# Optimization experiments

Measured on AMD Instinct MI355X. Metric: run time of the kernel, lower is better.

Reference implementation:

```python
import jax, jax.numpy as jnp
import numpy as np

N_NODES = 50000
N_EDGES = 800000
NODE_DIM = 128
EDGE_DIM = 10
IN_DIM = 2 * NODE_DIM + EDGE_DIM
BN_EPS = 1e-5


def setup_inputs() -> dict:
    key = jax.random.key(0)
    ks = jax.random.split(key, 8)
    h = jax.random.normal(ks[0], (N_NODES, NODE_DIM), dtype=jnp.float32)
    edge_index = jax.random.randint(ks[1], (2, N_EDGES), 0, N_NODES, dtype=jnp.int64)
    edge_feat = jax.random.normal(ks[2], (N_EDGES, EDGE_DIM), dtype=jnp.float32)
    scale = 1.0 / np.sqrt(IN_DIM)
    gate_w = jax.random.normal(ks[3], (IN_DIM, NODE_DIM), dtype=jnp.float32) * scale
    gate_b = jax.random.normal(ks[4], (NODE_DIM,), dtype=jnp.float32) * scale
    cand_w = jax.random.normal(ks[5], (IN_DIM, NODE_DIM), dtype=jnp.float32) * scale
    cand_b = jax.random.normal(ks[6], (NODE_DIM,), dtype=jnp.float32) * scale
    bn_gamma = jnp.ones((NODE_DIM,), dtype=jnp.float32)
    bn_beta = jnp.zeros((NODE_DIM,), dtype=jnp.float32)
    return {"h": h, "edge_index": edge_index, "edge_feat": edge_feat,
            "gate_w": gate_w, "gate_b": gate_b, "cand_w": cand_w, "cand_b": cand_b,
            "bn_gamma": bn_gamma, "bn_beta": bn_beta}


def reference(h, edge_index, edge_feat, gate_w, gate_b, cand_w, cand_b, bn_gamma, bn_beta):
    src = edge_index[0]
    dst = edge_index[1]
    # gather endpoint features and concat with edge features: [E, 2*D + De]
    z = jnp.concatenate([h[src], h[dst], edge_feat], axis=1)
    g = jax.nn.sigmoid(z @ gate_w + gate_b)   # [E, D]
    c = jax.nn.softplus(z @ cand_w + cand_b)  # [E, D]
    m = g * c
    # scatter-add messages to source nodes (matches index_add_(0, src, m))
    agg = jax.ops.segment_sum(m, src, num_segments=h.shape[0])
    # BatchNorm1d in training mode: batch mean / biased variance over nodes
    mean = jnp.mean(agg, axis=0)
    var = jnp.var(agg, axis=0)
    agg_bn = (agg - mean) * jax.lax.rsqrt(var + BN_EPS) * bn_gamma + bn_beta
    return jax.nn.softplus(h + agg_bn)
```

## Files before the change

### kernel.cpp

```cpp
#include <hip/hip_runtime.h>
#include <math.h>

#define N_NODES 50000
#define N_EDGES 800000
#define D 128
#define DE 10
#define TE 64
#define N_TILES (N_EDGES / TE)
#define SST 132
#define ASTR 136
#define OST 520
#define WP2_ELEMS (4 * 32 * 64 * 8)
#define WEF_ELEMS (16 * 64 * 8)
#define SCAN_BLOCKS 196
#define CSTRIDE 16

typedef __bf16 bf16x8 __attribute__((ext_vector_type(8)));
typedef __bf16 bf16x4 __attribute__((ext_vector_type(4)));
typedef __bf16 bf16x2 __attribute__((ext_vector_type(2)));
typedef float  f32x4  __attribute__((ext_vector_type(4)));

__device__ __forceinline__ float fast_sigmoid(float x) {
    float t = __builtin_amdgcn_exp2f(-1.44269504089f * x);
    return __builtin_amdgcn_rcpf(1.0f + t);
}
__device__ __forceinline__ float fast_softplus(float x) {
    float t = __builtin_amdgcn_exp2f(-1.44269504089f * fabsf(x));
    return fmaxf(x, 0.0f) + 0.69314718056f * __builtin_amdgcn_logf(1.0f + t);
}

__global__ __launch_bounds__(256) void prep(
    const float* __restrict__ gw, const float* __restrict__ cw,
    const int* __restrict__ ei,
    __bf16* __restrict__ wp2, __bf16* __restrict__ wef,
    int* __restrict__ counts)
{
    int bx = blockIdx.x, t = threadIdx.x;
    if (bx < 256) {
        int idx = bx * 256 + t;
        int j    = idx & 7;
        int lane = (idx >> 3) & 63;
        int nb   = (idx >> 9) & 31;
        int kb   = idx >> 14;
        int k    = kb * 32 + ((lane >> 4) << 3) + j;
        int jp   = nb * 16 + (lane & 15);
        float v;
        if      (jp < 128) v = gw[k * D + jp];
        else if (jp < 256) v = cw[k * D + (jp - 128)];
        else if (jp < 384) v = gw[(128 + k) * D + (jp - 256)];
        else               v = cw[(128 + k) * D + (jp - 384)];
        wp2[idx] = (__bf16)v;
    } else if (bx < 288) {
        int idx = (bx - 256) * 256 + t;
        int j    = idx & 7;
        int lane = (idx >> 3) & 63;
        int nb   = idx >> 9;
        int k    = ((lane >> 4) << 3) + j;
        int col  = (nb >> 1) * 16 + (lane & 15);
        const float* w = (nb & 1) ? cw : gw;
        wef[idx] = (__bf16)((k < 10) ? w[(256 + k) * D + col] : 0.0f);
    } else {
        int e = (bx - 288) * 256 + t;
        atomicAdd(&counts[ei[e] * CSTRIDE], 1);
    }
}

__global__ __launch_bounds__(256) void scan_partials(
    const int* __restrict__ counts, int* __restrict__ bsum)
{
    __shared__ int ss[256];
    int t = threadIdx.x;
    int i = blockIdx.x * 256 + t;
    int c = (i < N_NODES) ? counts[i * CSTRIDE] : 0;
    ss[t] = c;
    __syncthreads();
    #pragma unroll
    for (int off = 1; off < 256; off <<= 1) {
        int v = (t >= off) ? ss[t - off] : 0;
        __syncthreads();
        ss[t] += v;
        __syncthreads();
    }
    if (t == 255) bsum[blockIdx.x] = ss[255];
}

__global__ __launch_bounds__(256) void scan_final(
    int* __restrict__ counts, const int* __restrict__ bsum)
{
    __shared__ int sb[256];
    __shared__ int ss[256];
    int t = threadIdx.x;
    sb[t] = (t < SCAN_BLOCKS) ? bsum[t] : 0;
    int i = blockIdx.x * 256 + t;
    int c = (i < N_NODES) ? counts[i * CSTRIDE] : 0;
    ss[t] = c;
    __syncthreads();
    #pragma unroll
    for (int off = 1; off < 256; off <<= 1) {
        int v  = (t >= off) ? ss[t - off] : 0;
        int vb = (t >= off) ? sb[t - off] : 0;
        __syncthreads();
        ss[t] += v;
        sb[t] += vb;
        __syncthreads();
    }
    int base = blockIdx.x ? sb[blockIdx.x - 1] : 0;
    if (i < N_NODES) counts[i * CSTRIDE] = base + ss[t] - c;
}

__global__ __launch_bounds__(256) void csr_scatter(
    const int* __restrict__ ei, int* __restrict__ cursor,
    int2* __restrict__ sde)
{
    int e = blockIdx.x * 256 + threadIdx.x;
    int node = ei[e];
    int pos = atomicAdd(&cursor[node * CSTRIDE], 1);
    sde[pos] = make_int2(node | (ei[N_EDGES + e] << 16), e);
}

__global__ __launch_bounds__(512, 4) void node_gemm(
    const float* __restrict__ h, const __bf16* __restrict__ wp2,
    __bf16* __restrict__ pa, __bf16* __restrict__ pb)
{
    __shared__ __align__(16) __bf16 sm[64 * OST];
    __bf16* za = sm;
    const int t  = threadIdx.x;
    const int r0 = blockIdx.x * 64;

    #pragma unroll
    for (int it = 0; it < 4; ++it) {
        int ch  = it * 512 + t;
        int row = ch >> 5, cs = ch & 31;
        int node = r0 + row;
        float4 v = (node < N_NODES) ? *(const float4*)&h[(size_t)node * D + cs * 4]
                                    : make_float4(0.f, 0.f, 0.f, 0.f);
        bf16x4 o = { (__bf16)v.x, (__bf16)v.y, (__bf16)v.z, (__bf16)v.w };
        *(bf16x4*)&za[row * ASTR + cs * 4] = o;
    }
    __syncthreads();

    const int w = t >> 6, l = t & 63, quad = l >> 4, col16 = l & 15;
    f32x4 acc[4][4];
    #pragma unroll
    for (int mt = 0; mt < 4; ++mt)
        #pragma unroll
        for (int nt = 0; nt < 4; ++nt)
            acc[mt][nt] = (f32x4)0.0f;

    const __bf16* zp = &za[col16 * ASTR + quad * 8];
    const __bf16* bp = &wp2[(size_t)((w * 4) * 64 + l) * 8];

    #pragma unroll
    for (int kb = 0; kb < 4; ++kb) {
        bf16x8 afr[4];
        #pragma unroll
        for (int mt = 0; mt < 4; ++mt)
            afr[mt] = *(const bf16x8*)&zp[mt * 16 * ASTR + kb * 32];
        bf16x8 bfr[4];
        #pragma unroll
        for (int nt = 0; nt < 4; ++nt)
            bfr[nt] = *(const bf16x8*)&bp[(size_t)(kb * 32 + nt) * 512];
        #pragma unroll
        for (int mt = 0; mt < 4; ++mt)
            #pragma unroll
            for (int nt = 0; nt < 4; ++nt)
                acc[mt][nt] = __builtin_amdgcn_mfma_f32_16x16x32_bf16(
                    afr[mt], bfr[nt], acc[mt][nt], 0, 0, 0);
    }
    __syncthreads();

    #pragma unroll
    for (int mt = 0; mt < 4; ++mt)
        #pragma unroll
        for (int nt = 0; nt < 4; ++nt)
            #pragma unroll
            for (int r = 0; r < 4; ++r) {
                int row  = mt * 16 + quad * 4 + r;
                int colj = (w * 4 + nt) * 16 + col16;
                sm[row * OST + colj] = (__bf16)acc[mt][nt][r];
            }
    __syncthreads();

    #pragma unroll
    for (int it = 0; it < 8; ++it) {
        int ch  = it * 512 + t;
        int row = ch >> 6, cc = ch & 63;
        int node = r0 + row;
        if (node < N_NODES) {
            bf16x8 v = *(const bf16x8*)&sm[row * OST + cc * 8];
            int j0 = cc * 8;
            if (j0 < 256) *(bf16x8*)&pa[(size_t)node * 256 + j0]         = v;
            else          *(bf16x8*)&pb[(size_t)node * 256 + (j0 - 256)] = v;
        }
    }
}

__global__ __launch_bounds__(512, 6) void edge_fuse(
    const __bf16* __restrict__ pa, const __bf16* __restrict__ pb,
    const int2* __restrict__ sde, const float* __restrict__ ef,
    const __bf16* __restrict__ wef,
    const float* __restrict__ gb, const float* __restrict__ cb,
    float* __restrict__ agg)
{
    __shared__ __align__(16) unsigned int sbuf[TE * SST];
    __shared__ __align__(16) __bf16 zE[TE * 32];
    __shared__ int s_src[TE], s_dst[TE], s_eid[TE];

    const int t  = threadIdx.x;
    const int e0 = blockIdx.x * TE;
    const int w = t >> 6, l = t & 63, quad = l >> 4, col16 = l & 15;

    const __bf16* wpp = &wef[(size_t)((w * 2) * 64 + l) * 8];
    bf16x8 bfr0 = *(const bf16x8*)&wpp[0];
    bf16x8 bfr1 = *(const bf16x8*)&wpp[512];
    const int c = w * 16 + col16;
    const float gbv = gb[c], cbv = cb[c];

    if (t < TE) {
        int2 p = sde[e0 + t];
        s_src[t] = p.x & 0xFFFF;
        s_dst[t] = (p.x >> 16) & 0xFFFF;
        s_eid[t] = p.y;
    }
    __syncthreads();

    if (t < TE) {
        const float* efr = &ef[(size_t)s_eid[t] * DE];
        __bf16* row = &zE[t * 32];
        #pragma unroll
        for (int j = 0; j < 5; ++j) {
            float2 a = *(const float2*)&efr[j * 2];
            bf16x2 p = { (__bf16)a.x, (__bf16)a.y };
            *(bf16x2*)&row[j * 2] = p;
        }
        *(bf16x2*)&row[10] = (bf16x2)(__bf16)0.0f;
        *(bf16x4*)&row[12] = (bf16x4)(__bf16)0.0f;
        *(bf16x8*)&row[16] = (bf16x8)(__bf16)0.0f;
        *(bf16x8*)&row[24] = (bf16x8)(__bf16)0.0f;
    }

    #pragma unroll
    for (int it = 0; it < 2; ++it) {
        int id  = it * 512 + t;
        int e   = id >> 4, grp = id & 15;
        int src = s_src[e], dst = s_dst[e];
        int c0  = grp * 8;
        bf16x8 ag = *(const bf16x8*)&pa[(size_t)src * 256 + c0];
        bf16x8 ac = *(const bf16x8*)&pa[(size_t)src * 256 + 128 + c0];
        bf16x8 bg = *(const bf16x8*)&pb[(size_t)dst * 256 + c0];
        bf16x8 bc = *(const bf16x8*)&pb[(size_t)dst * 256 + 128 + c0];
        unsigned int wds[8];
        #pragma unroll
        for (int j = 0; j < 8; ++j) {
            float gs = (float)ag[j] + (float)bg[j];
            float cs = (float)ac[j] + (float)bc[j];
            bf16x2 pr = { (__bf16)gs, (__bf16)cs };
            wds[j] = __builtin_bit_cast(unsigned int, pr);
        }
        *(uint4*)&sbuf[e * SST + c0]     = *(const uint4*)&wds[0];
        *(uint4*)&sbuf[e * SST + c0 + 4] = *(const uint4*)&wds[4];
    }
    __syncthreads();

    f32x4 acc[4][2];
    #pragma unroll
    for (int mt = 0; mt < 4; ++mt) {
        const bf16x8 a = *(const bf16x8*)&zE[(mt * 16 + col16) * 32 + quad * 8];
        acc[mt][0] = __builtin_amdgcn_mfma_f32_16x16x32_bf16(a, bfr0, (f32x4)0.0f, 0, 0, 0);
        acc[mt][1] = __builtin_amdgcn_mfma_f32_16x16x32_bf16(a, bfr1, (f32x4)0.0f, 0, 0, 0);
    }

    #pragma unroll
    for (int mt = 0; mt < 4; ++mt) {
        #pragma unroll
        for (int r = 0; r < 4; ++r) {
            int e = mt * 16 + quad * 4 + r;
            unsigned int u = sbuf[e * SST + c];
            float gs = __builtin_bit_cast(float, u << 16);
            float cs = __builtin_bit_cast(float, u & 0xFFFF0000u);
            float sg = fast_sigmoid(acc[mt][0][r] + gs + gbv);
            float sp = fast_softplus(acc[mt][1][r] + cs + cbv);
            ((float*)sbuf)[e * SST + c] = sg * sp;
        }
    }
    __syncthreads();

    const int seg = t >> 7;
    const int cc  = t & 127;
    const int rlo = seg * 16, rhi = rlo + 16;
    int   cur = s_src[rlo];
    float s   = 0.0f;
    const float* ms = (const float*)sbuf;
    for (int e = rlo; e < rhi; ++e) {
        int node = s_src[e];
        float v  = ms[e * SST + cc];
        if (node != cur) {
            atomicAdd(&agg[(size_t)cur * D + cc], s);
            s = 0.0f; cur = node;
        }
        s += v;
    }
    atomicAdd(&agg[(size_t)cur * D + cc], s);
}

__global__ __launch_bounds__(256) void col_stats(
    const float* __restrict__ agg, float* __restrict__ stats)
{
    const int t    = threadIdx.x;
    const int col  = t & 127;
    const int half = t >> 7;
    float s = 0.0f, s2 = 0.0f;
    for (int r = blockIdx.x * 2 + half; r < N_NODES; r += gridDim.x * 2) {
        float v = agg[(size_t)r * D + col];
        s += v; s2 += v * v;
    }
    atomicAdd(&stats[col], s);
    atomicAdd(&stats[128 + col], s2);
}

__global__ __launch_bounds__(256) void out_softplus(
    const float* __restrict__ h, const float* __restrict__ agg,
    const float* __restrict__ stats, const float* __restrict__ gamma,
    const float* __restrict__ beta, float* __restrict__ out)
{
    __shared__ float sc[128], bi[128];
    int t = threadIdx.x;
    if (t < 128) {
        const float inv_n = 1.0f / (float)N_NODES;
        float mean = stats[t] * inv_n;
        float var  = stats[128 + t] * inv_n - mean * mean;
        var = fmaxf(var, 0.0f);
        float rstd = rsqrtf(var + 1e-5f);
        float s = rstd * gamma[t];
        sc[t] = s;
        bi[t] = beta[t] - mean * s;
    }
    __syncthreads();
    int idx4 = blockIdx.x * 256 + t;
    int base = idx4 * 4;
    if (base < N_NODES * D) {
        float4 hv = *(const float4*)&h[base];
        float4 av = *(const float4*)&agg[base];
        int c = base & 127;
        float4 o;
        o.x = fast_softplus(hv.x + av.x * sc[c + 0] + bi[c + 0]);
        o.y = fast_softplus(hv.y + av.y * sc[c + 1] + bi[c + 1]);
        o.z = fast_softplus(hv.z + av.z * sc[c + 2] + bi[c + 2]);
        o.w = fast_softplus(hv.w + av.w * sc[c + 3] + bi[c + 3]);
        *(float4*)&out[base] = o;
    }
}

extern "C" void kernel_launch(void* const* d_in, const int* in_sizes, int n_in,
                              void* d_out, int out_size, void* d_ws, size_t ws_size,
                              hipStream_t stream) {
    const float* h     = (const float*)d_in[0];
    const int*   ei    = (const int*)  d_in[1];
    const float* ef    = (const float*)d_in[2];
    const float* gw    = (const float*)d_in[3];
    const float* gb    = (const float*)d_in[4];
    const float* cw    = (const float*)d_in[5];
    const float* cb    = (const float*)d_in[6];
    const float* gamma = (const float*)d_in[7];
    const float* beta  = (const float*)d_in[8];
    float* out = (float*)d_out;

    float*  agg    = (float*)d_ws;
    float*  stats  = agg + (size_t)N_NODES * D;
    int*    counts = (int*)(stats + 256);
    int*    bsum   = counts + N_NODES * CSTRIDE;
    __bf16* pb     = (__bf16*)counts;
    char*   afterU = (char*)counts + (size_t)N_NODES * 256 * sizeof(__bf16);
    __bf16* wp2    = (__bf16*)afterU;
    __bf16* wef    = wp2 + WP2_ELEMS;
    int2*   sde    = (int2*)(wef + WEF_ELEMS);
    __bf16* pa     = (__bf16*)d_out;

    const size_t zero_bytes = ((size_t)N_NODES * D + 256) * sizeof(float)
                            + (size_t)N_NODES * CSTRIDE * sizeof(int);
    hipMemsetAsync(d_ws, 0, zero_bytes, stream);
    prep<<<3413, 256, 0, stream>>>(gw, cw, ei, wp2, wef, counts);
    scan_partials<<<SCAN_BLOCKS, 256, 0, stream>>>(counts, bsum);
    scan_final<<<SCAN_BLOCKS, 256, 0, stream>>>(counts, bsum);
    csr_scatter<<<N_EDGES / 256, 256, 0, stream>>>(ei, counts, sde);
    node_gemm<<<(N_NODES + 63) / 64, 512, 0, stream>>>(h, wp2, pa, pb);
    edge_fuse<<<N_TILES, 512, 0, stream>>>(pa, pb, sde, ef, wef, gb, cb, agg);
    col_stats<<<784, 256, 0, stream>>>(agg, stats);
    out_softplus<<<(N_NODES * D / 4 + 255) / 256, 256, 0, stream>>>(
        h, agg, stats, gamma, beta, out);
}
```

Baseline: 375.8 us.

## Replace edge-tiled MFMA fuse with per-node CSR wavefront aggregation without atomics

```diff
diff --git a/kernel.cpp b/kernel.cpp
--- a/kernel.cpp
+++ b/kernel.cpp
@@ -5,15 +5,11 @@
 #define N_EDGES 800000
 #define D 128
 #define DE 10
-#define TE 64
-#define N_TILES (N_EDGES / TE)
-#define SST 132
+#define WP2_ELEMS (4 * 32 * 64 * 8)
+#define SCAN_BLOCKS 196
+#define CSTRIDE 16
 #define ASTR 136
 #define OST 520
-#define WP2_ELEMS (4 * 32 * 64 * 8)
-#define WEF_ELEMS (16 * 64 * 8)
-#define SCAN_BLOCKS 196
-#define CSTRIDE 16
 
 typedef __bf16 bf16x8 __attribute__((ext_vector_type(8)));
 typedef __bf16 bf16x4 __attribute__((ext_vector_type(4)));
@@ -28,12 +24,17 @@
     float t = __builtin_amdgcn_exp2f(-1.44269504089f * fabsf(x));
     return fmaxf(x, 0.0f) + 0.69314718056f * __builtin_amdgcn_logf(1.0f + t);
 }
+__device__ __forceinline__ float2 bf2f(unsigned int u) {
+    float2 r;
+    r.x = __builtin_bit_cast(float, u << 16);
+    r.y = __builtin_bit_cast(float, u & 0xFFFF0000u);
+    return r;
+}
 
 __global__ __launch_bounds__(256) void prep(
     const float* __restrict__ gw, const float* __restrict__ cw,
     const int* __restrict__ ei,
-    __bf16* __restrict__ wp2, __bf16* __restrict__ wef,
-    int* __restrict__ counts)
+    __bf16* __restrict__ wp2, int* __restrict__ counts)
 {
     int bx = blockIdx.x, t = threadIdx.x;
     if (bx < 256) {
@@ -50,17 +51,8 @@
         else if (jp < 384) v = gw[(128 + k) * D + (jp - 256)];
         else               v = cw[(128 + k) * D + (jp - 384)];
         wp2[idx] = (__bf16)v;
-    } else if (bx < 288) {
-        int idx = (bx - 256) * 256 + t;
-        int j    = idx & 7;
-        int lane = (idx >> 3) & 63;
-        int nb   = idx >> 9;
-        int k    = ((lane >> 4) << 3) + j;
-        int col  = (nb >> 1) * 16 + (lane & 15);
-        const float* w = (nb & 1) ? cw : gw;
-        wef[idx] = (__bf16)((k < 10) ? w[(256 + k) * D + col] : 0.0f);
     } else {
-        int e = (bx - 288) * 256 + t;
+        int e = (bx - 256) * 256 + t;
         atomicAdd(&counts[ei[e] * CSTRIDE], 1);
     }
 }
@@ -85,7 +77,8 @@
 }
 
 __global__ __launch_bounds__(256) void scan_final(
-    int* __restrict__ counts, const int* __restrict__ bsum)
+    int* __restrict__ counts, const int* __restrict__ bsum,
+    int* __restrict__ rp)
 {
     __shared__ int sb[256];
     __shared__ int ss[256];
@@ -105,7 +98,12 @@
         __syncthreads();
     }
     int base = blockIdx.x ? sb[blockIdx.x - 1] : 0;
-    if (i < N_NODES) counts[i * CSTRIDE] = base + ss[t] - c;
+    if (i < N_NODES) {
+        int excl = base + ss[t] - c;
+        counts[i * CSTRIDE] = excl;
+        rp[i] = excl;
+    }
+    if (blockIdx.x == 0 && t == 0) rp[N_NODES] = N_EDGES;
 }
 
 __global__ __launch_bounds__(256) void csr_scatter(
@@ -115,7 +113,7 @@
     int e = blockIdx.x * 256 + threadIdx.x;
     int node = ei[e];
     int pos = atomicAdd(&cursor[node * CSTRIDE], 1);
-    sde[pos] = make_int2(node | (ei[N_EDGES + e] << 16), e);
+    sde[pos] = make_int2(ei[N_EDGES + e], e);
 }
 
 __global__ __launch_bounds__(512, 4) void node_gemm(
@@ -195,112 +193,66 @@
     }
 }
 
-__global__ __launch_bounds__(512, 6) void edge_fuse(
+__global__ __launch_bounds__(256, 6) void node_fuse(
     const __bf16* __restrict__ pa, const __bf16* __restrict__ pb,
     const int2* __restrict__ sde, const float* __restrict__ ef,
-    const __bf16* __restrict__ wef,
+    const int* __restrict__ rp,
+    const float* __restrict__ gw, const float* __restrict__ cw,
     const float* __restrict__ gb, const float* __restrict__ cb,
     float* __restrict__ agg)
 {
-    __shared__ __align__(16) unsigned int sbuf[TE * SST];
-    __shared__ __align__(16) __bf16 zE[TE * 32];
-    __shared__ int s_src[TE], s_dst[TE], s_eid[TE];
-
-    const int t  = threadIdx.x;
-    const int e0 = blockIdx.x * TE;
-    const int w = t >> 6, l = t & 63, quad = l >> 4, col16 = l & 15;
-
-    const __bf16* wpp = &wef[(size_t)((w * 2) * 64 + l) * 8];
-    bf16x8 bfr0 = *(const bf16x8*)&wpp[0];
-    bf16x8 bfr1 = *(const bf16x8*)&wpp[512];
-    const int c = w * 16 + col16;
-    const float gbv = gb[c], cbv = cb[c];
-
-    if (t < TE) {
-        int2 p = sde[e0 + t];
-        s_src[t] = p.x & 0xFFFF;
-        s_dst[t] = (p.x >> 16) & 0xFFFF;
-        s_eid[t] = p.y;
-    }
-    __syncthreads();
-
-    if (t < TE) {
-        const float* efr = &ef[(size_t)s_eid[t] * DE];
-        __bf16* row = &zE[t * 32];
-        #pragma unroll
-        for (int j = 0; j < 5; ++j) {
-            float2 a = *(const float2*)&efr[j * 2];
-            bf16x2 p = { (__bf16)a.x, (__bf16)a.y };
-            *(bf16x2*)&row[j * 2] = p;
+    const int t = threadIdx.x;
+    const int w = t >> 6, l = t & 63;
+    const int n = blockIdx.x * 4 + w;
+    const int c0 = 2 * l;
+
+    int beg = __builtin_amdgcn_readfirstlane(rp[n]);
+    int end = __builtin_amdgcn_readfirstlane(rp[n + 1]);
+
+    float2 ag = bf2f(*(const unsigned int*)&pa[(size_t)n * 256 + c0]);
+    float2 ac = bf2f(*(const unsigned int*)&pa[(size_t)n * 256 + 128 + c0]);
+
+    float4 wk[10];
+    #pragma unroll
+    for (int k = 0; k < 10; ++k) {
+        float2 g = *(const float2*)&gw[(size_t)(256 + k) * D + c0];
+        float2 c = *(const float2*)&cw[(size_t)(256 + k) * D + c0];
+        wk[k] = make_float4(g.x, g.y, c.x, c.y);
+    }
+    const float gb0 = gb[c0], gb1 = gb[c0 + 1];
+    const float cb0 = cb[c0], cb1 = cb[c0 + 1];
+
+    float acc0 = 0.0f, acc1 = 0.0f;
+
+    int2 rec = (beg < end) ? sde[beg] : make_int2(0, 0);
+    for (int i = beg; i < end; ++i) {
+        const int dst = __builtin_amdgcn_readfirstlane(rec.x);
+        const int eid = __builtin_amdgcn_readfirstlane(rec.y);
+        int2 nrec = (i + 1 < end) ? sde[i + 1] : rec;
+
+        unsigned int ugb = *(const unsigned int*)&pb[(size_t)dst * 256 + c0];
+        unsigned int ucb = *(const unsigned int*)&pb[(size_t)dst * 256 + 128 + c0];
+
+        const float* efr = &ef[(size_t)eid * DE];
+        float4 d = make_float4(gb0, gb1, cb0, cb1);
+        #pragma unroll
+        for (int k = 0; k < 10; ++k) {
+            float e = efr[k];
+            d.x = fmaf(e, wk[k].x, d.x);
+            d.y = fmaf(e, wk[k].y, d.y);
+            d.z = fmaf(e, wk[k].z, d.z);
+            d.w = fmaf(e, wk[k].w, d.w);
         }
-        *(bf16x2*)&row[10] = (bf16x2)(__bf16)0.0f;
-        *(bf16x4*)&row[12] = (bf16x4)(__bf16)0.0f;
-        *(bf16x8*)&row[16] = (bf16x8)(__bf16)0.0f;
-        *(bf16x8*)&row[24] = (bf16x8)(__bf16)0.0f;
-    }
-
-    #pragma unroll
-    for (int it = 0; it < 2; ++it) {
-        int id  = it * 512 + t;
-        int e   = id >> 4, grp = id & 15;
-        int src = s_src[e], dst = s_dst[e];
-        int c0  = grp * 8;
-        bf16x8 ag = *(const bf16x8*)&pa[(size_t)src * 256 + c0];
-        bf16x8 ac = *(const bf16x8*)&pa[(size_t)src * 256 + 128 + c0];
-        bf16x8 bg = *(const bf16x8*)&pb[(size_t)dst * 256 + c0];
-        bf16x8 bc = *(const bf16x8*)&pb[(size_t)dst * 256 + 128 + c0];
-        unsigned int wds[8];
-        #pragma unroll
-        for (int j = 0; j < 8; ++j) {
-            float gs = (float)ag[j] + (float)bg[j];
-            float cs = (float)ac[j] + (float)bc[j];
-            bf16x2 pr = { (__bf16)gs, (__bf16)cs };
-            wds[j] = __builtin_bit_cast(unsigned int, pr);
-        }
-        *(uint4*)&sbuf[e * SST + c0]     = *(const uint4*)&wds[0];
-        *(uint4*)&sbuf[e * SST + c0 + 4] = *(const uint4*)&wds[4];
-    }
-    __syncthreads();
-
-    f32x4 acc[4][2];
-    #pragma unroll
-    for (int mt = 0; mt < 4; ++mt) {
-        const bf16x8 a = *(const bf16x8*)&zE[(mt * 16 + col16) * 32 + quad * 8];
-        acc[mt][0] = __builtin_amdgcn_mfma_f32_16x16x32_bf16(a, bfr0, (f32x4)0.0f, 0, 0, 0);
-        acc[mt][1] = __builtin_amdgcn_mfma_f32_16x16x32_bf16(a, bfr1, (f32x4)0.0f, 0, 0, 0);
-    }
-
-    #pragma unroll
-    for (int mt = 0; mt < 4; ++mt) {
-        #pragma unroll
-        for (int r = 0; r < 4; ++r) {
-            int e = mt * 16 + quad * 4 + r;
-            unsigned int u = sbuf[e * SST + c];
-            float gs = __builtin_bit_cast(float, u << 16);
-            float cs = __builtin_bit_cast(float, u & 0xFFFF0000u);
-            float sg = fast_sigmoid(acc[mt][0][r] + gs + gbv);
-            float sp = fast_softplus(acc[mt][1][r] + cs + cbv);
-            ((float*)sbuf)[e * SST + c] = sg * sp;
-        }
-    }
-    __syncthreads();
-
-    const int seg = t >> 7;
-    const int cc  = t & 127;
-    const int rlo = seg * 16, rhi = rlo + 16;
-    int   cur = s_src[rlo];
-    float s   = 0.0f;
-    const float* ms = (const float*)sbuf;
-    for (int e = rlo; e < rhi; ++e) {
-        int node = s_src[e];
-        float v  = ms[e * SST + cc];
-        if (node != cur) {
-            atomicAdd(&agg[(size_t)cur * D + cc], s);
-            s = 0.0f; cur = node;
-        }
-        s += v;
-    }
-    atomicAdd(&agg[(size_t)cur * D + cc], s);
+        float2 bg = bf2f(ugb), bc = bf2f(ucb);
+        float g0 = ag.x + bg.x + d.x;
+        float g1 = ag.y + bg.y + d.y;
+        float x0 = ac.x + bc.x + d.z;
+        float x1 = ac.y + bc.y + d.w;
+        acc0 += fast_sigmoid(g0) * fast_softplus(x0);
+        acc1 += fast_sigmoid(g1) * fast_softplus(x1);
+        rec = nrec;
+    }
+    *(float2*)&agg[(size_t)n * D + c0] = make_float2(acc0, acc1);
 }
 
 __global__ __launch_bounds__(256) void col_stats(
@@ -372,20 +324,18 @@
     __bf16* pb     = (__bf16*)counts;
     char*   afterU = (char*)counts + (size_t)N_NODES * 256 * sizeof(__bf16);
     __bf16* wp2    = (__bf16*)afterU;
-    __bf16* wef    = wp2 + WP2_ELEMS;
-    int2*   sde    = (int2*)(wef + WEF_ELEMS);
+    int2*   sde    = (int2*)(wp2 + WP2_ELEMS);
+    int*    rp     = (int*)(sde + N_EDGES);
     __bf16* pa     = (__bf16*)d_out;
 
-    const size_t zero_bytes = ((size_t)N_NODES * D + 256) * sizeof(float)
-                            + (size_t)N_NODES * CSTRIDE * sizeof(int);
-    hipMemsetAsync(d_ws, 0, zero_bytes, stream);
-    prep<<<3413, 256, 0, stream>>>(gw, cw, ei, wp2, wef, counts);
+    hipMemsetAsync(stats, 0, 256 * sizeof(float) + (size_t)N_NODES * CSTRIDE * sizeof(int), stream);
+    prep<<<3381, 256, 0, stream>>>(gw, cw, ei, wp2, counts);
     scan_partials<<<SCAN_BLOCKS, 256, 0, stream>>>(counts, bsum);
-    scan_final<<<SCAN_BLOCKS, 256, 0, stream>>>(counts, bsum);
+    scan_final<<<SCAN_BLOCKS, 256, 0, stream>>>(counts, bsum, rp);
     csr_scatter<<<N_EDGES / 256, 256, 0, stream>>>(ei, counts, sde);
     node_gemm<<<(N_NODES + 63) / 64, 512, 0, stream>>>(h, wp2, pa, pb);
-    edge_fuse<<<N_TILES, 512, 0, stream>>>(pa, pb, sde, ef, wef, gb, cb, agg);
+    node_fuse<<<N_NODES / 4, 256, 0, stream>>>(pa, pb, sde, ef, rp, gw, cw, gb, cb, agg);
     col_stats<<<784, 256, 0, stream>>>(agg, stats);
-    out_softplus<<<(N_NODES * D / 4 + 255) / 256, 256, 0, stream>>>(
+    out_softplus<<<N_NODES * D / 4 / 256, 256, 0, stream>>>(
         h, agg, stats, gamma, beta, out);
 }
```

Result: slower. 426.8 us (+13.6%).

## Merge CSR build and BN finish stages into cooperative grid-synced kernels

Applied to the files above, without the earlier changes.

```diff
diff --git a/kernel.cpp b/kernel.cpp
--- a/kernel.cpp
+++ b/kernel.cpp
@@ -1,5 +1,8 @@
 #include <hip/hip_runtime.h>
+#include <hip/hip_cooperative_groups.h>
 #include <math.h>
+
+namespace cg = cooperative_groups;
 
 #define N_NODES 50000
 #define N_EDGES 800000
@@ -14,6 +17,7 @@
 #define WEF_ELEMS (16 * 64 * 8)
 #define SCAN_BLOCKS 196
 #define CSTRIDE 16
+#define ZERO_F4 1800064
 
 typedef __bf16 bf16x8 __attribute__((ext_vector_type(8)));
 typedef __bf16 bf16x4 __attribute__((ext_vector_type(4)));
@@ -29,15 +33,22 @@
     return fmaxf(x, 0.0f) + 0.69314718056f * __builtin_amdgcn_logf(1.0f + t);
 }
 
-__global__ __launch_bounds__(256) void prep(
+__global__ __launch_bounds__(256) void build_csr(
     const float* __restrict__ gw, const float* __restrict__ cw,
     const int* __restrict__ ei,
     __bf16* __restrict__ wp2, __bf16* __restrict__ wef,
-    int* __restrict__ counts)
+    int* __restrict__ counts, int* __restrict__ bsum,
+    int2* __restrict__ sde, float4* __restrict__ zbase)
 {
-    int bx = blockIdx.x, t = threadIdx.x;
-    if (bx < 256) {
-        int idx = bx * 256 + t;
+    cg::grid_group grid = cg::this_grid();
+    const int t = threadIdx.x, b = blockIdx.x;
+    const int gtid = b * 256 + t;
+    const int gstride = SCAN_BLOCKS * 256;
+
+    const float4 z4 = make_float4(0.f, 0.f, 0.f, 0.f);
+    for (int i = gtid; i < ZERO_F4; i += gstride)
+        zbase[i] = z4;
+    for (int idx = gtid; idx < WP2_ELEMS; idx += gstride) {
         int j    = idx & 7;
         int lane = (idx >> 3) & 63;
         int nb   = (idx >> 9) & 31;
@@ -50,8 +61,9 @@
         else if (jp < 384) v = gw[(128 + k) * D + (jp - 256)];
         else               v = cw[(128 + k) * D + (jp - 384)];
         wp2[idx] = (__bf16)v;
-    } else if (bx < 288) {
-        int idx = (bx - 256) * 256 + t;
+    }
+    if (gtid < WEF_ELEMS) {
+        int idx = gtid;
         int j    = idx & 7;
         int lane = (idx >> 3) & 63;
         int nb   = idx >> 9;
@@ -59,19 +71,18 @@
         int col  = (nb >> 1) * 16 + (lane & 15);
         const float* w = (nb & 1) ? cw : gw;
         wef[idx] = (__bf16)((k < 10) ? w[(256 + k) * D + col] : 0.0f);
-    } else {
-        int e = (bx - 288) * 256 + t;
+    }
+    grid.sync();
+
+    #pragma unroll 4
+    for (int e = gtid; e < N_EDGES; e += gstride)
         atomicAdd(&counts[ei[e] * CSTRIDE], 1);
-    }
-}
-
-__global__ __launch_bounds__(256) void scan_partials(
-    const int* __restrict__ counts, int* __restrict__ bsum)
-{
+    grid.sync();
+
     __shared__ int ss[256];
-    int t = threadIdx.x;
-    int i = blockIdx.x * 256 + t;
-    int c = (i < N_NODES) ? counts[i * CSTRIDE] : 0;
+    __shared__ int sb[256];
+    const int i = b * 256 + t;
+    const int c = (i < N_NODES) ? counts[i * CSTRIDE] : 0;
     ss[t] = c;
     __syncthreads();
     #pragma unroll
@@ -81,41 +92,28 @@
         ss[t] += v;
         __syncthreads();
     }
-    if (t == 255) bsum[blockIdx.x] = ss[255];
-}
-
-__global__ __launch_bounds__(256) void scan_final(
-    int* __restrict__ counts, const int* __restrict__ bsum)
-{
-    __shared__ int sb[256];
-    __shared__ int ss[256];
-    int t = threadIdx.x;
+    if (t == 255) bsum[b] = ss[255];
+    grid.sync();
+
     sb[t] = (t < SCAN_BLOCKS) ? bsum[t] : 0;
-    int i = blockIdx.x * 256 + t;
-    int c = (i < N_NODES) ? counts[i * CSTRIDE] : 0;
-    ss[t] = c;
     __syncthreads();
     #pragma unroll
     for (int off = 1; off < 256; off <<= 1) {
-        int v  = (t >= off) ? ss[t - off] : 0;
-        int vb = (t >= off) ? sb[t - off] : 0;
+        int v = (t >= off) ? sb[t - off] : 0;
         __syncthreads();
-        ss[t] += v;
-        sb[t] += vb;
+        sb[t] += v;
         __syncthreads();
     }
-    int base = blockIdx.x ? sb[blockIdx.x - 1] : 0;
+    int base = b ? sb[b - 1] : 0;
     if (i < N_NODES) counts[i * CSTRIDE] = base + ss[t] - c;
-}
-
-__global__ __launch_bounds__(256) void csr_scatter(
-    const int* __restrict__ ei, int* __restrict__ cursor,
-    int2* __restrict__ sde)
-{
-    int e = blockIdx.x * 256 + threadIdx.x;
-    int node = ei[e];
-    int pos = atomicAdd(&cursor[node * CSTRIDE], 1);
-    sde[pos] = make_int2(node | (ei[N_EDGES + e] << 16), e);
+    grid.sync();
+
+    #pragma unroll 4
+    for (int e = gtid; e < N_EDGES; e += gstride) {
+        int node = ei[e];
+        int pos = atomicAdd(&counts[node * CSTRIDE], 1);
+        sde[pos] = make_int2(node | (ei[N_EDGES + e] << 16), e);
+    }
 }
 
 __global__ __launch_bounds__(512, 4) void node_gemm(
@@ -303,28 +301,28 @@
     atomicAdd(&agg[(size_t)cur * D + cc], s);
 }
 
-__global__ __launch_bounds__(256) void col_stats(
-    const float* __restrict__ agg, float* __restrict__ stats)
-{
-    const int t    = threadIdx.x;
-    const int col  = t & 127;
-    const int half = t >> 7;
-    float s = 0.0f, s2 = 0.0f;
-    for (int r = blockIdx.x * 2 + half; r < N_NODES; r += gridDim.x * 2) {
-        float v = agg[(size_t)r * D + col];
-        s += v; s2 += v * v;
-    }
-    atomicAdd(&stats[col], s);
-    atomicAdd(&stats[128 + col], s2);
-}
-
-__global__ __launch_bounds__(256) void out_softplus(
+__global__ __launch_bounds__(256) void finish(
     const float* __restrict__ h, const float* __restrict__ agg,
-    const float* __restrict__ stats, const float* __restrict__ gamma,
+    float* __restrict__ stats, const float* __restrict__ gamma,
     const float* __restrict__ beta, float* __restrict__ out)
 {
+    cg::grid_group grid = cg::this_grid();
+    const int t = threadIdx.x;
+
+    {
+        const int col  = t & 127;
+        const int half = t >> 7;
+        float s = 0.0f, s2 = 0.0f;
+        for (int r = blockIdx.x * 2 + half; r < N_NODES; r += gridDim.x * 2) {
+            float v = agg[(size_t)r * D + col];
+            s += v; s2 += v * v;
+        }
+        atomicAdd(&stats[col], s);
+        atomicAdd(&stats[128 + col], s2);
+    }
+    grid.sync();
+
     __shared__ float sc[128], bi[128];
-    int t = threadIdx.x;
     if (t < 128) {
         const float inv_n = 1.0f / (float)N_NODES;
         float mean = stats[t] * inv_n;
@@ -336,17 +334,17 @@
         bi[t] = beta[t] - mean * s;
     }
     __syncthreads();
-    int idx4 = blockIdx.x * 256 + t;
-    int base = idx4 * 4;
-    if (base < N_NODES * D) {
+    const int total4 = N_NODES * D / 4;
+    for (int idx4 = blockIdx.x * 256 + t; idx4 < total4; idx4 += gridDim.x * 256) {
+        int base = idx4 * 4;
         float4 hv = *(const float4*)&h[base];
         float4 av = *(const float4*)&agg[base];
-        int c = base & 127;
+        int cc = base & 127;
         float4 o;
-        o.x = fast_softplus(hv.x + av.x * sc[c + 0] + bi[c + 0]);
-        o.y = fast_softplus(hv.y + av.y * sc[c + 1] + bi[c + 1]);
-        o.z = fast_softplus(hv.z + av.z * sc[c + 2] + bi[c + 2]);
-        o.w = fast_softplus(hv.w + av.w * sc[c + 3] + bi[c + 3]);
+        o.x = fast_softplus(hv.x + av.x * sc[cc + 0] + bi[cc + 0]);
+        o.y = fast_softplus(hv.y + av.y * sc[cc + 1] + bi[cc + 1]);
+        o.z = fast_softplus(hv.z + av.z * sc[cc + 2] + bi[cc + 2]);
+        o.w = fast_softplus(hv.w + av.w * sc[cc + 3] + bi[cc + 3]);
         *(float4*)&out[base] = o;
     }
 }
@@ -375,17 +373,21 @@
     __bf16* wef    = wp2 + WP2_ELEMS;
     int2*   sde    = (int2*)(wef + WEF_ELEMS);
     __bf16* pa     = (__bf16*)d_out;
-
-    const size_t zero_bytes = ((size_t)N_NODES * D + 256) * sizeof(float)
-                            + (size_t)N_NODES * CSTRIDE * sizeof(int);
-    hipMemsetAsync(d_ws, 0, zero_bytes, stream);
-    prep<<<3413, 256, 0, stream>>>(gw, cw, ei, wp2, wef, counts);
-    scan_partials<<<SCAN_BLOCKS, 256, 0, stream>>>(counts, bsum);
-    scan_final<<<SCAN_BLOCKS, 256, 0, stream>>>(counts, bsum);
-    csr_scatter<<<N_EDGES / 256, 256, 0, stream>>>(ei, counts, sde);
+    float4* zbase  = (float4*)d_ws;
+
+    {
+        void* args[] = { (void*)&gw, (void*)&cw, (void*)&ei, (void*)&wp2,
+                         (void*)&wef, (void*)&counts, (void*)&bsum,
+                         (void*)&sde, (void*)&zbase };
+        hipLaunchCooperativeKernel((const void*)build_csr,
+                                   dim3(SCAN_BLOCKS), dim3(256), args, 0, stream);
+    }
     node_gemm<<<(N_NODES + 63) / 64, 512, 0, stream>>>(h, wp2, pa, pb);
     edge_fuse<<<N_TILES, 512, 0, stream>>>(pa, pb, sde, ef, wef, gb, cb, agg);
-    col_stats<<<784, 256, 0, stream>>>(agg, stats);
-    out_softplus<<<(N_NODES * D / 4 + 255) / 256, 256, 0, stream>>>(
-        h, agg, stats, gamma, beta, out);
-}
+    {
+        void* args[] = { (void*)&h, (void*)&agg, (void*)&stats,
+                         (void*)&gamma, (void*)&beta, (void*)&out };
+        hipLaunchCooperativeKernel((const void*)finish,
+                                   dim3(784), dim3(256), args, 0, stream);
+    }
+}
```

After: 519.9 us. 38.3% more time.

## Replace atomic CSR scatter with rank-based permutation and interleave gate/cand projections

Applied to the files above, without the earlier changes.

```diff
diff --git a/kernel.cpp b/kernel.cpp
--- a/kernel.cpp
+++ b/kernel.cpp
@@ -14,6 +14,8 @@
 #define WEF_ELEMS (16 * 64 * 8)
 #define SCAN_BLOCKS 196
 #define CSTRIDE 16
+#define SCAT_BLOCKS 1563
+#define GEMM_BLOCKS 782
 
 typedef __bf16 bf16x8 __attribute__((ext_vector_type(8)));
 typedef __bf16 bf16x4 __attribute__((ext_vector_type(4)));
@@ -28,12 +30,18 @@
     float t = __builtin_amdgcn_exp2f(-1.44269504089f * fabsf(x));
     return fmaxf(x, 0.0f) + 0.69314718056f * __builtin_amdgcn_logf(1.0f + t);
 }
+__device__ __forceinline__ float bflo(unsigned int u) {
+    return __builtin_bit_cast(float, u << 16);
+}
+__device__ __forceinline__ float bfhi(unsigned int u) {
+    return __builtin_bit_cast(float, u & 0xFFFF0000u);
+}
 
 __global__ __launch_bounds__(256) void prep(
     const float* __restrict__ gw, const float* __restrict__ cw,
     const int* __restrict__ ei,
     __bf16* __restrict__ wp2, __bf16* __restrict__ wef,
-    int* __restrict__ counts)
+    int* __restrict__ counts, unsigned short* __restrict__ rank)
 {
     int bx = blockIdx.x, t = threadIdx.x;
     if (bx < 256) {
@@ -61,7 +69,8 @@
         wef[idx] = (__bf16)((k < 10) ? w[(256 + k) * D + col] : 0.0f);
     } else {
         int e = (bx - 288) * 256 + t;
-        atomicAdd(&counts[ei[e] * CSTRIDE], 1);
+        int r = atomicAdd(&counts[ei[e] * CSTRIDE], 1);
+        rank[e] = (unsigned short)r;
     }
 }
 
@@ -85,7 +94,8 @@
 }
 
 __global__ __launch_bounds__(256) void scan_final(
-    int* __restrict__ counts, const int* __restrict__ bsum)
+    const int* __restrict__ counts, const int* __restrict__ bsum,
+    int* __restrict__ excl)
 {
     __shared__ int sb[256];
     __shared__ int ss[256];
@@ -105,27 +115,28 @@
         __syncthreads();
     }
     int base = blockIdx.x ? sb[blockIdx.x - 1] : 0;
-    if (i < N_NODES) counts[i * CSTRIDE] = base + ss[t] - c;
-}
-
-__global__ __launch_bounds__(256) void csr_scatter(
-    const int* __restrict__ ei, int* __restrict__ cursor,
-    int2* __restrict__ sde)
-{
-    int e = blockIdx.x * 256 + threadIdx.x;
-    int node = ei[e];
-    int pos = atomicAdd(&cursor[node * CSTRIDE], 1);
-    sde[pos] = make_int2(node | (ei[N_EDGES + e] << 16), e);
-}
-
-__global__ __launch_bounds__(512, 4) void node_gemm(
+    if (i < N_NODES) excl[i] = base + ss[t] - c;
+}
+
+__global__ __launch_bounds__(512, 4) void scatter_gemm(
+    const int* __restrict__ ei, const unsigned short* __restrict__ rank,
+    const int* __restrict__ excl, int* __restrict__ perm,
     const float* __restrict__ h, const __bf16* __restrict__ wp2,
-    __bf16* __restrict__ pa, __bf16* __restrict__ pb)
-{
+    unsigned int* __restrict__ paI, unsigned int* __restrict__ pbI)
+{
+    if (blockIdx.x < SCAT_BLOCKS) {
+        int e = blockIdx.x * 512 + threadIdx.x;
+        if (e < N_EDGES) {
+            int node = ei[e];
+            perm[excl[node] + (int)rank[e]] = e;
+        }
+        return;
+    }
+
     __shared__ __align__(16) __bf16 sm[64 * OST];
     __bf16* za = sm;
     const int t  = threadIdx.x;
-    const int r0 = blockIdx.x * 64;
+    const int r0 = (blockIdx.x - SCAT_BLOCKS) * 64;
 
     #pragma unroll
     for (int it = 0; it < 4; ++it) {
@@ -183,28 +194,38 @@
 
     #pragma unroll
     for (int it = 0; it < 8; ++it) {
-        int ch  = it * 512 + t;
-        int row = ch >> 6, cc = ch & 63;
+        int ch   = it * 512 + t;
+        int row  = ch >> 6;
+        int sub  = ch & 63;
+        int hp   = sub >> 5;
+        int c0   = (sub & 31) * 4;
         int node = r0 + row;
         if (node < N_NODES) {
-            bf16x8 v = *(const bf16x8*)&sm[row * OST + cc * 8];
-            int j0 = cc * 8;
-            if (j0 < 256) *(bf16x8*)&pa[(size_t)node * 256 + j0]         = v;
-            else          *(bf16x8*)&pb[(size_t)node * 256 + (j0 - 256)] = v;
+            const __bf16* sr = &sm[row * OST + hp * 256];
+            bf16x4 gl = *(const bf16x4*)&sr[c0];
+            bf16x4 cl = *(const bf16x4*)&sr[128 + c0];
+            unsigned int wds[4];
+            #pragma unroll
+            for (int i = 0; i < 4; ++i) {
+                bf16x2 pr = { gl[i], cl[i] };
+                wds[i] = __builtin_bit_cast(unsigned int, pr);
+            }
+            unsigned int* dp = hp ? pbI : paI;
+            *(uint4*)&dp[(size_t)node * 128 + c0] = *(const uint4*)&wds[0];
         }
     }
 }
 
 __global__ __launch_bounds__(512, 6) void edge_fuse(
-    const __bf16* __restrict__ pa, const __bf16* __restrict__ pb,
-    const int2* __restrict__ sde, const float* __restrict__ ef,
-    const __bf16* __restrict__ wef,
+    const unsigned int* __restrict__ paI, const unsigned int* __restrict__ pbI,
+    const int* __restrict__ perm, const int* __restrict__ ei,
+    const float* __restrict__ ef, const __bf16* __restrict__ wef,
     const float* __restrict__ gb, const float* __restrict__ cb,
     float* __restrict__ agg)
 {
-    __shared__ __align__(16) unsigned int sbuf[TE * SST];
+    __shared__ __align__(16) float ms[TE * SST];
     __shared__ __align__(16) __bf16 zE[TE * 32];
-    __shared__ int s_src[TE], s_dst[TE], s_eid[TE];
+    __shared__ int s_src[TE], s_dst[TE];
 
     const int t  = threadIdx.x;
     const int e0 = blockIdx.x * TE;
@@ -217,49 +238,22 @@
     const float gbv = gb[c], cbv = cb[c];
 
     if (t < TE) {
-        int2 p = sde[e0 + t];
-        s_src[t] = p.x & 0xFFFF;
-        s_dst[t] = (p.x >> 16) & 0xFFFF;
-        s_eid[t] = p.y;
-    }
-    __syncthreads();
-
-    if (t < TE) {
-        const float* efr = &ef[(size_t)s_eid[t] * DE];
+        int p = perm[e0 + t];
+        s_src[t] = ei[p];
+        s_dst[t] = ei[N_EDGES + p];
+        const float* efr = &ef[(size_t)p * DE];
         __bf16* row = &zE[t * 32];
         #pragma unroll
         for (int j = 0; j < 5; ++j) {
             float2 a = *(const float2*)&efr[j * 2];
-            bf16x2 p = { (__bf16)a.x, (__bf16)a.y };
-            *(bf16x2*)&row[j * 2] = p;
+            bf16x2 pr = { (__bf16)a.x, (__bf16)a.y };
+            *(bf16x2*)&row[j * 2] = pr;
         }
         *(bf16x2*)&row[10] = (bf16x2)(__bf16)0.0f;
         *(bf16x4*)&row[12] = (bf16x4)(__bf16)0.0f;
         *(bf16x8*)&row[16] = (bf16x8)(__bf16)0.0f;
         *(bf16x8*)&row[24] = (bf16x8)(__bf16)0.0f;
     }
-
-    #pragma unroll
-    for (int it = 0; it < 2; ++it) {
-        int id  = it * 512 + t;
-        int e   = id >> 4, grp = id & 15;
-        int src = s_src[e], dst = s_dst[e];
-        int c0  = grp * 8;
-        bf16x8 ag = *(const bf16x8*)&pa[(size_t)src * 256 + c0];
-        bf16x8 ac = *(const bf16x8*)&pa[(size_t)src * 256 + 128 + c0];
-        bf16x8 bg = *(const bf16x8*)&pb[(size_t)dst * 256 + c0];
-        bf16x8 bc = *(const bf16x8*)&pb[(size_t)dst * 256 + 128 + c0];
-        unsigned int wds[8];
-        #pragma unroll
-        for (int j = 0; j < 8; ++j) {
-            float gs = (float)ag[j] + (float)bg[j];
-            float cs = (float)ac[j] + (float)bc[j];
-            bf16x2 pr = { (__bf16)gs, (__bf16)cs };
-            wds[j] = __builtin_bit_cast(unsigned int, pr);
-        }
-        *(uint4*)&sbuf[e * SST + c0]     = *(const uint4*)&wds[0];
-        *(uint4*)&sbuf[e * SST + c0 + 4] = *(const uint4*)&wds[4];
-    }
     __syncthreads();
 
     f32x4 acc[4][2];
@@ -272,15 +266,19 @@
 
     #pragma unroll
     for (int mt = 0; mt < 4; ++mt) {
+        unsigned int uA[4], uB[4];
         #pragma unroll
         for (int r = 0; r < 4; ++r) {
             int e = mt * 16 + quad * 4 + r;
-            unsigned int u = sbuf[e * SST + c];
-            float gs = __builtin_bit_cast(float, u << 16);
-            float cs = __builtin_bit_cast(float, u & 0xFFFF0000u);
-            float sg = fast_sigmoid(acc[mt][0][r] + gs + gbv);
-            float sp = fast_softplus(acc[mt][1][r] + cs + cbv);
-            ((float*)sbuf)[e * SST + c] = sg * sp;
+            uA[r] = paI[(size_t)s_src[e] * 128 + c];
+            uB[r] = pbI[(size_t)s_dst[e] * 128 + c];
+        }
+        #pragma unroll
+        for (int r = 0; r < 4; ++r) {
+            int e = mt * 16 + quad * 4 + r;
+            float g = bflo(uA[r]) + bflo(uB[r]) + acc[mt][0][r] + gbv;
+            float x = bfhi(uA[r]) + bfhi(uB[r]) + acc[mt][1][r] + cbv;
+            ms[e * SST + c] = fast_sigmoid(g) * fast_softplus(x);
         }
     }
     __syncthreads();
@@ -290,7 +288,6 @@
     const int rlo = seg * 16, rhi = rlo + 16;
     int   cur = s_src[rlo];
     float s   = 0.0f;
-    const float* ms = (const float*)sbuf;
     for (int e = rlo; e < rhi; ++e) {
         int node = s_src[e];
         float v  = ms[e * SST + cc];
@@ -365,27 +362,29 @@
     const float* beta  = (const float*)d_in[8];
     float* out = (float*)d_out;
 
-    float*  agg    = (float*)d_ws;
-    float*  stats  = agg + (size_t)N_NODES * D;
-    int*    counts = (int*)(stats + 256);
-    int*    bsum   = counts + N_NODES * CSTRIDE;
-    __bf16* pb     = (__bf16*)counts;
-    char*   afterU = (char*)counts + (size_t)N_NODES * 256 * sizeof(__bf16);
-    __bf16* wp2    = (__bf16*)afterU;
-    __bf16* wef    = wp2 + WP2_ELEMS;
-    int2*   sde    = (int2*)(wef + WEF_ELEMS);
-    __bf16* pa     = (__bf16*)d_out;
+    float*          agg    = (float*)d_ws;
+    float*          stats  = agg + (size_t)N_NODES * D;
+    int*            counts = (int*)(stats + 256);
+    unsigned int*   pbI    = (unsigned int*)counts;
+    char*           afterU = (char*)counts + (size_t)N_NODES * 128 * sizeof(unsigned int);
+    __bf16*         wp2    = (__bf16*)afterU;
+    __bf16*         wef    = wp2 + WP2_ELEMS;
+    int*            bsum   = (int*)(wef + WEF_ELEMS);
+    int*            excl   = bsum + 256;
+    unsigned short* rank   = (unsigned short*)(excl + N_NODES);
+    int*            perm   = (int*)(rank + N_EDGES);
+    unsigned int*   paI    = (unsigned int*)d_out;
 
     const size_t zero_bytes = ((size_t)N_NODES * D + 256) * sizeof(float)
                             + (size_t)N_NODES * CSTRIDE * sizeof(int);
     hipMemsetAsync(d_ws, 0, zero_bytes, stream);
-    prep<<<3413, 256, 0, stream>>>(gw, cw, ei, wp2, wef, counts);
+    prep<<<3413, 256, 0, stream>>>(gw, cw, ei, wp2, wef, counts, rank);
     scan_partials<<<SCAN_BLOCKS, 256, 0, stream>>>(counts, bsum);
-    scan_final<<<SCAN_BLOCKS, 256, 0, stream>>>(counts, bsum);
-    csr_scatter<<<N_EDGES / 256, 256, 0, stream>>>(ei, counts, sde);
-    node_gemm<<<(N_NODES + 63) / 64, 512, 0, stream>>>(h, wp2, pa, pb);
-    edge_fuse<<<N_TILES, 512, 0, stream>>>(pa, pb, sde, ef, wef, gb, cb, agg);
+    scan_final<<<SCAN_BLOCKS, 256, 0, stream>>>(counts, bsum, excl);
+    scatter_gemm<<<SCAT_BLOCKS + GEMM_BLOCKS, 512, 0, stream>>>(
+        ei, rank, excl, perm, h, wp2, paI, pbI);
+    edge_fuse<<<N_TILES, 512, 0, stream>>>(paI, pbI, perm, ei, ef, wef, gb, cb, agg);
     col_stats<<<784, 256, 0, stream>>>(agg, stats);
-    out_softplus<<<(N_NODES * D / 4 + 255) / 256, 256, 0, stream>>>(
+    out_softplus<<<N_NODES * D / 4 / 256, 256, 0, stream>>>(
         h, agg, stats, gamma, beta, out);
 }
```

Measured after the change: 346.5 us. 1.08x faster.
